# Optimization experiments

Measured on AMD Instinct MI355X. Metric: run time of the kernel, lower is better.

Reference implementation:

```python
import jax, jax.numpy as jnp
import numpy as np

N = 12288   # nodes
E = 393216  # edges (avg degree 32)
B = 16      # graphs in batch
F_IN = 15   # node feature dim
H = 32      # hidden_dim
EMB = 64    # embedding_dim
NC = 11     # num_classes
EDIM = 2    # edge feature dim
EPS = 1e-5  # BatchNorm eps


def _bn(x, gamma, beta):
    # training-mode BatchNorm1d: biased batch variance, matches torch normalization
    mu = jnp.mean(x, axis=0)
    var = jnp.var(x, axis=0)
    return gamma * (x - mu) * jax.lax.rsqrt(var + EPS) + beta


def setup_inputs() -> dict:
    key = jax.random.key(0)
    ks = jax.random.split(key, 16)
    def p(k, shape, s=0.05):
        return jax.random.normal(k, shape, dtype=jnp.float32) * s
    z = lambda *s: jnp.zeros(s, jnp.float32)
    o = lambda *s: jnp.ones(s, jnp.float32)
    return {
        "x": jax.random.normal(ks[0], (N, F_IN), dtype=jnp.float32),
        "edge_attr": jax.random.normal(ks[1], (E, EDIM), dtype=jnp.float32),
        "w_edge": p(ks[2], (EDIM, 1)), "b_edge": z(1),
        "w1": p(ks[3], (F_IN, H)), "b1": z(H), "g1": o(H), "be1": z(H),
        "w2": p(ks[4], (H, 2 * H)), "b2": z(2 * H), "g2": o(2 * H), "be2": z(2 * H),
        "w3": p(ks[5], (2 * H, EMB)), "b3": z(EMB), "g3": o(EMB), "be3": z(EMB),
        "wf1": p(ks[6], (EMB, 512)), "bf1": z(512), "gf1": o(512), "bef1": z(512),
        "wf2": p(ks[7], (512, 256)), "bf2": z(256), "gf2": o(256), "bef2": z(256),
        "wf3": p(ks[8], (256, NC)), "bf3": z(NC),
        "edge_index": jax.random.randint(ks[9], (2, E), 0, N, dtype=jnp.int64)
                      if jax.config.jax_enable_x64 else jax.random.randint(ks[9], (2, E), 0, N),
        "batch": jnp.sort(jax.random.randint(ks[10], (N,), 0, B)),
    }


def reference(x, edge_attr, w_edge, b_edge,
              w1, b1, g1, be1, w2, b2, g2, be2, w3, b3, g3, be3,
              wf1, bf1, gf1, bef1, wf2, bf2, gf2, bef2, wf3, bf3,
              edge_index, batch):
    # edge weights: sigmoid(Linear(edge_attr)) -> [E]
    ew = jax.nn.sigmoid(edge_attr @ w_edge + b_edge)[:, 0]
    # dense adjacency with self loops, accumulate duplicates (sparse_coo.to_dense)
    loop = jnp.arange(N)
    row = jnp.concatenate([edge_index[0], loop])
    col = jnp.concatenate([edge_index[1], loop])
    w_aug = jnp.concatenate([ew, jnp.ones((N,), ew.dtype)])
    adj = jnp.zeros((N, N), ew.dtype).at[row, col].add(w_aug)
    # symmetric degree normalization D^-1/2 A D^-1/2
    deg = adj.sum(axis=1)
    dis = jnp.where(deg > 0, jax.lax.rsqrt(jnp.where(deg > 0, deg, 1.0)), 0.0)
    support = dis[:, None] * adj * dis[None, :]
    # three GCN layers: support @ x @ W + b, BN, relu
    h = jax.nn.relu(_bn(support @ x @ w1 + b1, g1, be1))
    h = jax.nn.relu(_bn(support @ h @ w2 + b2, g2, be2))
    h = jax.nn.relu(_bn(support @ h @ w3 + b3, g3, be3))
    # global max pool per graph (empty graphs -> zeros)
    seg = jax.ops.segment_max(h, batch, num_segments=B)
    cnt = jax.ops.segment_sum(jnp.ones((N,), h.dtype), batch, num_segments=B)
    emb = jnp.where(cnt[:, None] > 0, seg, 0.0)
    # MLP head (dropout = identity at inference)
    o = jax.nn.relu(_bn(emb @ wf1 + bf1, gf1, bef1))
    o = jax.nn.relu(_bn(o @ wf2 + bf2, gf2, bef2))
    logits = o @ wf3 + bf3
    return jax.nn.log_softmax(logits, axis=1), emb
```

## Files before the change

### kernel.cpp

```cpp
#include <hip/hip_runtime.h>
#include <hip/hip_bf16.h>

#define NN   12288
#define EE   393216
#define WELL 128
#define NELL (NN*WELL)
#define BG   16
#define FIN  15
#define FH1  32
#define FH2  64
#define NCL  11
#define BNEPS 1e-5f
#define NBANK 32

typedef unsigned long long u64;
static inline int cdiv(long a, long b){ return (int)((a + b - 1) / b); }

__device__ __forceinline__ int getIdx(const void* p, long i, int is64){
  return is64 ? (int)((const long long*)p)[i] : ((const int*)p)[i];
}

__global__ void k_pre(u64* deg_cnt, float* csp1, float* csp2, float* csp3,
                      float* embf, const void* ei, const void* batch, int* flags){
  int g = blockIdx.x*256 + threadIdx.x;
  if (g < NN) deg_cnt[g] = 0ull;
  if (g < NBANK*128){ csp1[g] = 0.f; csp2[g] = 0.f; csp3[g] = 0.f; }
  if (g < BG*64) embf[g] = 0.f;
  if (blockIdx.x == 0 && threadIdx.x < 64){
    const int* a = (const int*)ei;
    unsigned long long m0 = __ballot(a[2*threadIdx.x + 1] == 0);
    const int* b = (const int*)batch;
    int j = 96*threadIdx.x;
    unsigned long long m1 = __ballot(b[2*j + 1] == 0);
    if (threadIdx.x == 0){
      flags[0] = (m0 == ~0ull) ? 1 : 0;
      flags[1] = (m1 == ~0ull) ? 1 : 0;
    }
  }
}

__global__ void k_edge(const float* ea, const float* we, const float* bedg,
                       const void* ei, const int* flags, u64* deg_cnt, u64* csr_p){
  int e = blockIdx.x*256 + threadIdx.x;
  if (e >= EE) return;
  int is64 = flags[0];
  float2 eav = ((const float2*)ea)[e];
  float z = eav.x*we[0] + eav.y*we[1] + bedg[0];
  float w = 1.0f/(1.0f + expf(-z));
  int r = getIdx(ei, e, is64);
  int c = getIdx(ei, (long)EE + e, is64);
  u64 add = (1ull << 32) | (u64)__float2uint_rn(w * 1048576.0f);
  u64 old = atomicAdd(&deg_cnt[r], add);
  int slot = (int)(old >> 32);
  if (slot < WELL)
    csr_p[((long)r << 7) + slot] = (u64)(unsigned)c | ((u64)__float_as_uint(w) << 32);
}

__global__ void k_dis(const u64* __restrict__ deg_cnt, float* __restrict__ dis){
  int g = blockIdx.x*256 + threadIdx.x;
  if (g < NN){
    unsigned lo = (unsigned)(deg_cnt[g] & 0xffffffffull);
    dis[g] = rsqrtf(1.0f + (float)lo * (1.0f/1048576.0f));
  }
}

template<int F, int FP, int FO, int APPLY_BN>
__global__ void __launch_bounds__(256) k_layer(
    const float* __restrict__ Hin,
    const float* __restrict__ cspin, const float* __restrict__ gam,
    const float* __restrict__ bet,
    const float* __restrict__ W, const float* __restrict__ bias,
    const u64* __restrict__ deg_cnt, const u64* __restrict__ csr_p,
    const float* __restrict__ dis,
    float* __restrict__ Pout, float* __restrict__ csout){
  const int R = 256/FP;
  __shared__ float At[R][FP];
  __shared__ float lcs[FO], lcq[FO];
  __shared__ float lsc[64], lsh[64];
  if (threadIdx.x < FO){ lcs[threadIdx.x] = 0.f; lcq[threadIdx.x] = 0.f; }
  if (APPLY_BN && threadIdx.x < F){
    float s = 0.f, q = 0.f;
    #pragma unroll
    for (int b = 0; b < NBANK; b++){
      s += cspin[b*128 + threadIdx.x];
      q += cspin[b*128 + 64 + threadIdx.x];
    }
    float mu  = s*(1.0f/NN);
    float var = q*(1.0f/NN) - mu*mu;
    float sc = gam[threadIdx.x]*rsqrtf(var + BNEPS);
    lsc[threadIdx.x] = sc;
    lsh[threadIdx.x] = bet[threadIdx.x] - mu*sc;
  }
  __syncthreads();
  int f = threadIdx.x % FP, lr = threadIdx.x / FP;
  float sc = 1.f, sh = 0.f;
  if (APPLY_BN && f < F){ sc = lsc[f]; sh = lsh[f]; }
  int row = blockIdx.x*R + lr;
  if (f < F){
    float d = dis[row];
    int n = (int)(deg_cnt[row] >> 32);
    n = n < WELL ? n : WELL;
    float v0 = Hin[row*F + f];
    if (APPLY_BN) v0 = fmaxf(v0*sc + sh, 0.f);
    float acc = d * v0;
    int nch = (n + 7) >> 3;
    const uint4* pb = (const uint4*)(csr_p + ((long)row << 7));
    if (nch > 0){
      uint4 a0 = pb[0], a1 = pb[1], a2 = pb[2], a3 = pb[3];
      for (int ch = 0; ch < nch; ch++){
        uint4 b0, b1, b2, b3;
        bool more = (ch + 1 < nch);
        if (more){ b0 = pb[4*ch+4]; b1 = pb[4*ch+5]; b2 = pb[4*ch+6]; b3 = pb[4*ch+7]; }
        int base = ch*8;
        if (base + 8 > n){
          if (base+0 >= n){ a0.x = 0u; a0.y = 0u; }
          if (base+1 >= n){ a0.z = 0u; a0.w = 0u; }
          if (base+2 >= n){ a1.x = 0u; a1.y = 0u; }
          if (base+3 >= n){ a1.z = 0u; a1.w = 0u; }
          if (base+4 >= n){ a2.x = 0u; a2.y = 0u; }
          if (base+5 >= n){ a2.z = 0u; a2.w = 0u; }
          if (base+6 >= n){ a3.x = 0u; a3.y = 0u; }
          if (base+7 >= n){ a3.z = 0u; a3.w = 0u; }
        }
        float w0 = __uint_as_float(a0.y) * dis[(int)a0.x];
        float w1 = __uint_as_float(a0.w) * dis[(int)a0.z];
        float w2 = __uint_as_float(a1.y) * dis[(int)a1.x];
        float w3 = __uint_as_float(a1.w) * dis[(int)a1.z];
        float w4 = __uint_as_float(a2.y) * dis[(int)a2.x];
        float w5 = __uint_as_float(a2.w) * dis[(int)a2.z];
        float w6 = __uint_as_float(a3.y) * dis[(int)a3.x];
        float w7 = __uint_as_float(a3.w) * dis[(int)a3.z];
        float h0 = Hin[(int)a0.x*F + f];
        float h1 = Hin[(int)a0.z*F + f];
        float h2 = Hin[(int)a1.x*F + f];
        float h3 = Hin[(int)a1.z*F + f];
        float h4 = Hin[(int)a2.x*F + f];
        float h5 = Hin[(int)a2.z*F + f];
        float h6 = Hin[(int)a3.x*F + f];
        float h7 = Hin[(int)a3.z*F + f];
        if (APPLY_BN){
          h0 = fmaxf(h0*sc + sh, 0.f); h1 = fmaxf(h1*sc + sh, 0.f);
          h2 = fmaxf(h2*sc + sh, 0.f); h3 = fmaxf(h3*sc + sh, 0.f);
          h4 = fmaxf(h4*sc + sh, 0.f); h5 = fmaxf(h5*sc + sh, 0.f);
          h6 = fmaxf(h6*sc + sh, 0.f); h7 = fmaxf(h7*sc + sh, 0.f);
        }
        acc += w0*h0 + w1*h1 + w2*h2 + w3*h3
             + w4*h4 + w5*h5 + w6*h6 + w7*h7;
        if (more){ a0 = b0; a1 = b1; a2 = b2; a3 = b3; }
      }
    }
    At[lr][f] = d * acc;
  }
  __syncthreads();
  const int fo = threadIdx.x % FO;
  float bb = bias[fo];
  for (int o = threadIdx.x; o < R*FO; o += 256){
    int l = o / FO;
    float s = bb;
    #pragma unroll
    for (int fi = 0; fi < F; fi++) s += At[l][fi] * W[fi*FO + fo];
    Pout[(blockIdx.x*R + l)*FO + fo] = s;
    atomicAdd(&lcs[fo], s);
    atomicAdd(&lcq[fo], s*s);
  }
  __syncthreads();
  if (threadIdx.x < FO){
    int bank = blockIdx.x & (NBANK-1);
    atomicAdd(&csout[bank*128 + threadIdx.x],      lcs[threadIdx.x]);
    atomicAdd(&csout[bank*128 + 64 + threadIdx.x], lcq[threadIdx.x]);
  }
}

__global__ void k_pool(const float* P3, const float* csp, const float* gam,
                       const float* bet, const void* batch, const int* flags,
                       float* embf){
  __shared__ float lsc[64], lsh[64];
  if (threadIdx.x < 64){
    float s = 0.f, q = 0.f;
    #pragma unroll
    for (int b = 0; b < NBANK; b++){
      s += csp[b*128 + threadIdx.x];
      q += csp[b*128 + 64 + threadIdx.x];
    }
    float mu  = s*(1.0f/NN);
    float var = q*(1.0f/NN) - mu*mu;
    float sc = gam[threadIdx.x]*rsqrtf(var + BNEPS);
    lsc[threadIdx.x] = sc;
    lsh[threadIdx.x] = bet[threadIdx.x] - mu*sc;
  }
  __syncthreads();
  int is64 = flags[1];
  int b = blockIdx.x & 15, chunk = blockIdx.x >> 4;
  int lo = 0, hi = NN;
  while (lo < hi){ int m = (lo+hi)>>1; if (getIdx(batch, m, is64) < b) lo = m+1; else hi = m; }
  int start = lo;
  lo = start; hi = NN;
  while (lo < hi){ int m = (lo+hi)>>1; if (getIdx(batch, m, is64) < b+1) lo = m+1; else hi = m; }
  int end = lo;
  int f = threadIdx.x & 63, grp = threadIdx.x >> 6;
  float sc = lsc[f], sh = lsh[f];
  float m = 0.0f;
  for (int i = start + chunk*4 + grp; i < end; i += 64)
    m = fmaxf(m, P3[(long)i*FH2 + f]*sc + sh);
  __shared__ float shm[4][64];
  shm[grp][f] = m;
  __syncthreads();
  if (grp == 0){
    float v = fmaxf(fmaxf(shm[0][f], shm[1][f]), fmaxf(shm[2][f], shm[3][f]));
    atomicMax((int*)&embf[b*64 + f], __float_as_int(v));
  }
}

__global__ void __launch_bounds__(256) k_fcA(const float* embf, const float* wf1,
    const float* bf1, const float* gf1, const float* bef1, float* s1g, float* out){
  if (blockIdx.x == 0){
    #pragma unroll
    for (int i = 0; i < 4; i++)
      out[BG*NCL + i*256 + threadIdx.x] = embf[i*256 + threadIdx.x];
  }
  int c = blockIdx.x*4 + (threadIdx.x >> 6);
  int l = threadIdx.x & 63;
  float wcol = wf1[l*512 + c];
  float z[BG];
  #pragma unroll
  for (int r = 0; r < BG; r++){
    float v = embf[r*64 + l] * wcol;
    #pragma unroll
    for (int off = 32; off > 0; off >>= 1) v += __shfl_down(v, off);
    z[r] = v;
  }
  if (l == 0){
    float bb = bf1[c];
    float s = 0.f, q = 0.f;
    #pragma unroll
    for (int r = 0; r < BG; r++){ float zr = z[r] + bb; s += zr; q += zr*zr; }
    float mean = s*(1.f/BG), var = q*(1.f/BG) - mean*mean;
    float inv = rsqrtf(var + BNEPS);
    float gg = gf1[c], b2 = bef1[c];
    #pragma unroll
    for (int r = 0; r < BG; r++)
      s1g[r*512 + c] = fmaxf(gg*(z[r] + bb - mean)*inv + b2, 0.f);
  }
}

__global__ void __launch_bounds__(256) k_fcB(const float* s1g, const float* wf2,
    const float* bf2, const float* gf2, const float* bef2, float* s2g){
  int c = blockIdx.x*4 + (threadIdx.x >> 6);
  int l = threadIdx.x & 63;
  float wreg[8];
  #pragma unroll
  for (int j = 0; j < 8; j++) wreg[j] = wf2[(l + 64*j)*256 + c];
  float z[BG];
  #pragma unroll
  for (int r = 0; r < BG; r++){
    float v = 0.f;
    #pragma unroll
    for (int j = 0; j < 8; j++) v += s1g[r*512 + l + 64*j] * wreg[j];
    #pragma unroll
    for (int off = 32; off > 0; off >>= 1) v += __shfl_down(v, off);
    z[r] = v;
  }
  if (l == 0){
    float bb = bf2[c];
    float s = 0.f, q = 0.f;
    #pragma unroll
    for (int r = 0; r < BG; r++){ float zr = z[r] + bb; s += zr; q += zr*zr; }
    float mean = s*(1.f/BG), var = q*(1.f/BG) - mean*mean;
    float inv = rsqrtf(var + BNEPS);
    float gg = gf2[c], b2 = bef2[c];
    #pragma unroll
    for (int r = 0; r < BG; r++)
      s2g[r*256 + c] = fmaxf(gg*(z[r] + bb - mean)*inv + b2, 0.f);
  }
}

__global__ void k_fc3(const float* s2g, const float* wf3, const float* bf3, float* out){
  __shared__ float s2[BG*256];
  __shared__ float sl[BG*NCL];
  int t = threadIdx.x;
  for (int i = t; i < BG*256; i += 256) s2[i] = s2g[i];
  __syncthreads();
  if (t < BG*NCL){
    int r = t / NCL, c = t - r*NCL;
    float s = bf3[c];
    for (int k = 0; k < 256; k++) s += s2[r*256 + k]*wf3[k*NCL + c];
    sl[t] = s;
  }
  __syncthreads();
  if (t < BG){
    float m = -1e30f;
    for (int c = 0; c < NCL; c++) m = fmaxf(m, sl[t*NCL + c]);
    float s = 0.f;
    for (int c = 0; c < NCL; c++) s += expf(sl[t*NCL + c] - m);
    float lg = logf(s) + m;
    for (int c = 0; c < NCL; c++) out[t*NCL + c] = sl[t*NCL + c] - lg;
  }
}

extern "C" void kernel_launch(void* const* d_in, const int* in_sizes, int n_in,
                              void* d_out, int out_size, void* d_ws, size_t ws_size,
                              hipStream_t stream){
  const float* x    = (const float*)d_in[0];
  const float* ea   = (const float*)d_in[1];
  const float* we   = (const float*)d_in[2];
  const float* bedg = (const float*)d_in[3];
  const float* w1   = (const float*)d_in[4];  const float* b1  = (const float*)d_in[5];
  const float* g1   = (const float*)d_in[6];  const float* be1 = (const float*)d_in[7];
  const float* w2   = (const float*)d_in[8];  const float* b2  = (const float*)d_in[9];
  const float* g2   = (const float*)d_in[10]; const float* be2 = (const float*)d_in[11];
  const float* w3   = (const float*)d_in[12]; const float* b3  = (const float*)d_in[13];
  const float* g3   = (const float*)d_in[14]; const float* be3 = (const float*)d_in[15];
  const float* wf1  = (const float*)d_in[16]; const float* bf1 = (const float*)d_in[17];
  const float* gf1  = (const float*)d_in[18]; const float* bef1= (const float*)d_in[19];
  const float* wf2  = (const float*)d_in[20]; const float* bf2 = (const float*)d_in[21];
  const float* gf2  = (const float*)d_in[22]; const float* bef2= (const float*)d_in[23];
  const float* wf3  = (const float*)d_in[24]; const float* bf3 = (const float*)d_in[25];
  const void* ei    = d_in[26];
  const void* batch = d_in[27];
  float* out = (float*)d_out;

  u64* wq = (u64*)d_ws;
  u64* deg_cnt = wq; wq += NN;
  u64* csr_p   = wq; wq += NELL;
  float* ws = (float*)wq;
  float* P1    = ws; ws += NN*FH1;
  float* P2    = ws; ws += NN*FH2;
  float* P3    = ws; ws += NN*FH2;
  float* csp1  = ws; ws += NBANK*128;
  float* csp2  = ws; ws += NBANK*128;
  float* csp3  = ws; ws += NBANK*128;
  float* dis   = ws; ws += NN;
  float* embf  = ws; ws += BG*64;
  float* s1g   = ws; ws += BG*512;
  float* s2g   = ws; ws += BG*256;
  int* flags   = (int*)ws;

  k_pre<<<48, 256, 0, stream>>>(deg_cnt, csp1, csp2, csp3, embf, ei, batch, flags);
  k_edge<<<cdiv(EE,256), 256, 0, stream>>>(ea, we, bedg, ei, flags, deg_cnt, csr_p);
  k_dis<<<48, 256, 0, stream>>>(deg_cnt, dis);

  k_layer<FIN,16,FH1,0><<<NN/16, 256, 0, stream>>>(x, nullptr, nullptr, nullptr,
      w1, b1, deg_cnt, csr_p, dis, P1, csp1);
  k_layer<FH1,32,FH2,1><<<NN/8, 256, 0, stream>>>(P1, csp1, g1, be1,
      w2, b2, deg_cnt, csr_p, dis, P2, csp2);
  k_layer<FH2,64,FH2,1><<<NN/4, 256, 0, stream>>>(P2, csp2, g2, be2,
      w3, b3, deg_cnt, csr_p, dis, P3, csp3);

  k_pool<<<256, 256, 0, stream>>>(P3, csp3, g3, be3, batch, flags, embf);
  k_fcA<<<128, 256, 0, stream>>>(embf, wf1, bf1, gf1, bef1, s1g, out);
  k_fcB<<<64, 256, 0, stream>>>(s1g, wf2, bf2, gf2, bef2, s2g);
  k_fc3<<<1, 256, 0, stream>>>(s2g, wf3, bf3, out);
}
```

Measured before the change: 233.9 us.

## Fuse degree normalization into layer kernels and widen edge chunk to 16

Removes the separate k_dis kernel and dis buffer. Each layer now computes rsqrt of the degree on the fly, reading the low 32 bits of deg_cnt for the row and for every neighbor. The neighbor loop also processes 16 edges per chunk with array-based prefetch instead of 8, for more memory-level parallelism. The trade-off is one fewer launch against recomputing rsqrt per edge in three layers, more registers, and neighbor reads that come from the 8-byte-strided deg_cnt array rather than a packed float array.

```diff
diff --git a/kernel.cpp b/kernel.cpp
--- a/kernel.cpp
+++ b/kernel.cpp
@@ -18,6 +18,10 @@
 
 __device__ __forceinline__ int getIdx(const void* p, long i, int is64){
   return is64 ? (int)((const long long*)p)[i] : ((const int*)p)[i];
+}
+
+__device__ __forceinline__ float degOf(unsigned lo){
+  return 1.0f + (float)lo * (1.0f/1048576.0f);
 }
 
 __global__ void k_pre(u64* deg_cnt, float* csp1, float* csp2, float* csp3,
@@ -56,14 +60,6 @@
     csr_p[((long)r << 7) + slot] = (u64)(unsigned)c | ((u64)__float_as_uint(w) << 32);
 }
 
-__global__ void k_dis(const u64* __restrict__ deg_cnt, float* __restrict__ dis){
-  int g = blockIdx.x*256 + threadIdx.x;
-  if (g < NN){
-    unsigned lo = (unsigned)(deg_cnt[g] & 0xffffffffull);
-    dis[g] = rsqrtf(1.0f + (float)lo * (1.0f/1048576.0f));
-  }
-}
-
 template<int F, int FP, int FO, int APPLY_BN>
 __global__ void __launch_bounds__(256) k_layer(
     const float* __restrict__ Hin,
@@ -71,7 +67,6 @@
     const float* __restrict__ bet,
     const float* __restrict__ W, const float* __restrict__ bias,
     const u64* __restrict__ deg_cnt, const u64* __restrict__ csr_p,
-    const float* __restrict__ dis,
     float* __restrict__ Pout, float* __restrict__ csout){
   const int R = 256/FP;
   __shared__ float At[R][FP];
@@ -96,57 +91,52 @@
   float sc = 1.f, sh = 0.f;
   if (APPLY_BN && f < F){ sc = lsc[f]; sh = lsh[f]; }
   int row = blockIdx.x*R + lr;
+  const unsigned* __restrict__ cl = (const unsigned*)deg_cnt;
   if (f < F){
-    float d = dis[row];
-    int n = (int)(deg_cnt[row] >> 32);
+    u64 dc = deg_cnt[row];
+    float d = rsqrtf(degOf((unsigned)(dc & 0xffffffffull)));
+    int n = (int)(dc >> 32);
     n = n < WELL ? n : WELL;
     float v0 = Hin[row*F + f];
     if (APPLY_BN) v0 = fmaxf(v0*sc + sh, 0.f);
     float acc = d * v0;
-    int nch = (n + 7) >> 3;
+    int nch = (n + 15) >> 4;
     const uint4* pb = (const uint4*)(csr_p + ((long)row << 7));
     if (nch > 0){
-      uint4 a0 = pb[0], a1 = pb[1], a2 = pb[2], a3 = pb[3];
+      uint4 a[8], b[8];
+      #pragma unroll
+      for (int j = 0; j < 8; j++) a[j] = pb[j];
       for (int ch = 0; ch < nch; ch++){
-        uint4 b0, b1, b2, b3;
         bool more = (ch + 1 < nch);
-        if (more){ b0 = pb[4*ch+4]; b1 = pb[4*ch+5]; b2 = pb[4*ch+6]; b3 = pb[4*ch+7]; }
-        int base = ch*8;
-        if (base + 8 > n){
-          if (base+0 >= n){ a0.x = 0u; a0.y = 0u; }
-          if (base+1 >= n){ a0.z = 0u; a0.w = 0u; }
-          if (base+2 >= n){ a1.x = 0u; a1.y = 0u; }
-          if (base+3 >= n){ a1.z = 0u; a1.w = 0u; }
-          if (base+4 >= n){ a2.x = 0u; a2.y = 0u; }
-          if (base+5 >= n){ a2.z = 0u; a2.w = 0u; }
-          if (base+6 >= n){ a3.x = 0u; a3.y = 0u; }
-          if (base+7 >= n){ a3.z = 0u; a3.w = 0u; }
+        if (more){
+          #pragma unroll
+          for (int j = 0; j < 8; j++) b[j] = pb[8*ch + 8 + j];
         }
-        float w0 = __uint_as_float(a0.y) * dis[(int)a0.x];
-        float w1 = __uint_as_float(a0.w) * dis[(int)a0.z];
-        float w2 = __uint_as_float(a1.y) * dis[(int)a1.x];
-        float w3 = __uint_as_float(a1.w) * dis[(int)a1.z];
-        float w4 = __uint_as_float(a2.y) * dis[(int)a2.x];
-        float w5 = __uint_as_float(a2.w) * dis[(int)a2.z];
-        float w6 = __uint_as_float(a3.y) * dis[(int)a3.x];
-        float w7 = __uint_as_float(a3.w) * dis[(int)a3.z];
-        float h0 = Hin[(int)a0.x*F + f];
-        float h1 = Hin[(int)a0.z*F + f];
-        float h2 = Hin[(int)a1.x*F + f];
-        float h3 = Hin[(int)a1.z*F + f];
-        float h4 = Hin[(int)a2.x*F + f];
-        float h5 = Hin[(int)a2.z*F + f];
-        float h6 = Hin[(int)a3.x*F + f];
-        float h7 = Hin[(int)a3.z*F + f];
-        if (APPLY_BN){
-          h0 = fmaxf(h0*sc + sh, 0.f); h1 = fmaxf(h1*sc + sh, 0.f);
-          h2 = fmaxf(h2*sc + sh, 0.f); h3 = fmaxf(h3*sc + sh, 0.f);
-          h4 = fmaxf(h4*sc + sh, 0.f); h5 = fmaxf(h5*sc + sh, 0.f);
-          h6 = fmaxf(h6*sc + sh, 0.f); h7 = fmaxf(h7*sc + sh, 0.f);
+        int base = ch*16;
+        if (base + 16 > n){
+          #pragma unroll
+          for (int j = 0; j < 8; j++){
+            if (base + 2*j     >= n){ a[j].x = 0u; a[j].y = 0u; }
+            if (base + 2*j + 1 >= n){ a[j].z = 0u; a[j].w = 0u; }
+          }
         }
-        acc += w0*h0 + w1*h1 + w2*h2 + w3*h3
-             + w4*h4 + w5*h5 + w6*h6 + w7*h7;
-        if (more){ a0 = b0; a1 = b1; a2 = b2; a3 = b3; }
+        #pragma unroll
+        for (int j = 0; j < 8; j++){
+          int c0 = (int)a[j].x, c1 = (int)a[j].z;
+          float w0 = __uint_as_float(a[j].y) * rsqrtf(degOf(cl[2*c0]));
+          float w1 = __uint_as_float(a[j].w) * rsqrtf(degOf(cl[2*c1]));
+          float h0 = Hin[c0*F + f];
+          float h1 = Hin[c1*F + f];
+          if (APPLY_BN){
+            h0 = fmaxf(h0*sc + sh, 0.f);
+            h1 = fmaxf(h1*sc + sh, 0.f);
+          }
+          acc += w0*h0 + w1*h1;
+        }
+        if (more){
+          #pragma unroll
+          for (int j = 0; j < 8; j++) a[j] = b[j];
+        }
       }
     }
     At[lr][f] = d * acc;
@@ -329,7 +319,6 @@
   float* csp1  = ws; ws += NBANK*128;
   float* csp2  = ws; ws += NBANK*128;
   float* csp3  = ws; ws += NBANK*128;
-  float* dis   = ws; ws += NN;
   float* embf  = ws; ws += BG*64;
   float* s1g   = ws; ws += BG*512;
   float* s2g   = ws; ws += BG*256;
@@ -337,14 +326,13 @@
 
   k_pre<<<48, 256, 0, stream>>>(deg_cnt, csp1, csp2, csp3, embf, ei, batch, flags);
   k_edge<<<cdiv(EE,256), 256, 0, stream>>>(ea, we, bedg, ei, flags, deg_cnt, csr_p);
-  k_dis<<<48, 256, 0, stream>>>(deg_cnt, dis);
 
   k_layer<FIN,16,FH1,0><<<NN/16, 256, 0, stream>>>(x, nullptr, nullptr, nullptr,
-      w1, b1, deg_cnt, csr_p, dis, P1, csp1);
+      w1, b1, deg_cnt, csr_p, P1, csp1);
   k_layer<FH1,32,FH2,1><<<NN/8, 256, 0, stream>>>(P1, csp1, g1, be1,
-      w2, b2, deg_cnt, csr_p, dis, P2, csp2);
+      w2, b2, deg_cnt, csr_p, P2, csp2);
   k_layer<FH2,64,FH2,1><<<NN/4, 256, 0, stream>>>(P2, csp2, g2, be2,
-      w3, b3, deg_cnt, csr_p, dis, P3, csp3);
+      w3, b3, deg_cnt, csr_p, P3, csp3);
 
   k_pool<<<256, 256, 0, stream>>>(P3, csp3, g3, be3, batch, flags, embf);
   k_fcA<<<128, 256, 0, stream>>>(embf, wf1, bf1, gf1, bef1, s1g, out);
```

Result: no change. 238.0 us (+1.8%).
